# Performance work log

Hardware: AMD Instinct MI355X
Metric: run time of the kernel (lower is better)

The kernel has to match this reference:

```python
import jax, jax.numpy as jnp
import numpy as np

N_HEADS = 16
N_KV_HEADS = 4
HEAD_DIM = 128


def _rope(x, cos, sin):
    # x: [b, s, h, d]; cos/sin: [s, d//2]; interleaved pair rotation
    b, s, h, d = x.shape
    xp = x.reshape(b, s, h, d // 2, 2)
    x_r, x_i = xp[..., 0], xp[..., 1]
    c = cos[None, :, None, :]
    sn = sin[None, :, None, :]
    o_r = x_r * c - x_i * sn
    o_i = x_r * sn + x_i * c
    return jnp.stack([o_r, o_i], axis=-1).reshape(b, s, h, d)


def setup_inputs() -> dict:
    key = jax.random.key(0)
    ks = jax.random.split(key, 7)
    B, S, D = 2, 2048, 2048
    KV = N_KV_HEADS * HEAD_DIM
    x = jax.random.normal(ks[0], (B, S, D), dtype=jnp.float32)
    freqs_cos = jax.random.uniform(ks[1], (S, HEAD_DIM // 2), dtype=jnp.float32)
    freqs_sin = jax.random.uniform(ks[2], (S, HEAD_DIM // 2), dtype=jnp.float32)
    scale = 0.02
    wq = jax.random.normal(ks[3], (D, D), dtype=jnp.float32) * scale
    wk = jax.random.normal(ks[4], (KV, D), dtype=jnp.float32) * scale
    wv = jax.random.normal(ks[5], (KV, D), dtype=jnp.float32) * scale
    wo = jax.random.normal(ks[6], (D, D), dtype=jnp.float32) * scale
    return {"x": x, "freqs_cos": freqs_cos, "freqs_sin": freqs_sin,
            "wq": wq, "wk": wk, "wv": wv, "wo": wo}


def reference(x, freqs_cos, freqs_sin, wq, wk, wv, wo):
    B, S, D = x.shape
    n_rep = N_HEADS // N_KV_HEADS
    q = (x @ wq.T).reshape(B, S, N_HEADS, HEAD_DIM)
    k = (x @ wk.T).reshape(B, S, N_KV_HEADS, HEAD_DIM)
    v = (x @ wv.T).reshape(B, S, N_KV_HEADS, HEAD_DIM)
    q = _rope(q, freqs_cos, freqs_sin)
    k = _rope(k, freqs_cos, freqs_sin)
    # repeat_kv == torch.repeat_interleave along head dim
    k = jnp.repeat(k, n_rep, axis=2)
    v = jnp.repeat(v, n_rep, axis=2)
    q = q.transpose(0, 2, 1, 3)  # [B, H, S, d]
    k = k.transpose(0, 2, 1, 3)
    v = v.transpose(0, 2, 1, 3)
    scale = 1.0 / np.sqrt(HEAD_DIM).astype(np.float32)
    scores = jnp.einsum('bhqd,bhkd->bhqk', q, k) * scale
    causal = jnp.tril(jnp.ones((S, S), dtype=bool))
    scores = jnp.where(causal[None, None], scores, jnp.finfo(jnp.float32).min)
    probs = jax.nn.softmax(scores.astype(jnp.float32), axis=-1).astype(q.dtype)
    out = jnp.einsum('bhqk,bhkd->bhqd', probs, v)
    out = out.transpose(0, 2, 1, 3).reshape(B, S, N_HEADS * HEAD_DIM)
    return out @ wo.T
```

## Files before the change

kernel.cpp:

```cpp
#include <hip/hip_runtime.h>
#include <hip/hip_bf16.h>
#include <type_traits>

using bf16x8 = __attribute__((ext_vector_type(8))) short;
using f32x4  = __attribute__((ext_vector_type(4))) float;
using u16x8  = __attribute__((ext_vector_type(8))) unsigned short;
using u16x4  = __attribute__((ext_vector_type(4))) unsigned short;
using u32x4  = __attribute__((ext_vector_type(4))) unsigned int;

__device__ __forceinline__ float b2f(unsigned short u) {
    unsigned int x = ((unsigned int)u) << 16;
    return __builtin_bit_cast(float, x);
}
__device__ __forceinline__ unsigned short f2b(float f) {
    __hip_bfloat16 h = __float2bfloat16(f);
    return __builtin_bit_cast(unsigned short, h);
}

#if defined(__has_builtin)
#if __has_builtin(__builtin_amdgcn_exp2f)
#define EXP2F(x) __builtin_amdgcn_exp2f(x)
#else
#define EXP2F(x) exp2f(x)
#endif
#else
#define EXP2F(x) exp2f(x)
#endif

__device__ __forceinline__ void async_copy16(const void* g, void* l) {
    __builtin_amdgcn_global_load_lds(
        (const __attribute__((address_space(1))) unsigned int*)g,
        (__attribute__((address_space(3))) unsigned int*)l, 16, 0, 0);
}

#define MFMA16(a, b, c) __builtin_amdgcn_mfma_f32_16x16x32_bf16(a, b, c, 0, 0, 0)

#define BARRIER() do { asm volatile("" ::: "memory"); \
    __builtin_amdgcn_s_barrier(); asm volatile("" ::: "memory"); } while (0)
#define VMCNT6() asm volatile("s_waitcnt vmcnt(6)" ::: "memory")
#define VMCNT0() asm volatile("s_waitcnt vmcnt(0)" ::: "memory")

__global__ __launch_bounds__(256) void cvt_all(
    const float* __restrict__ x,  const float* __restrict__ wq,
    const float* __restrict__ wk, const float* __restrict__ wv,
    const float* __restrict__ wo,
    unsigned short* __restrict__ xb,  unsigned short* __restrict__ wqb,
    unsigned short* __restrict__ wkb, unsigned short* __restrict__ wvb,
    unsigned short* __restrict__ wob)
{
    int i = blockIdx.x * 256 + threadIdx.x;
    const float* s; unsigned short* d; int j;
    if (i < 2097152)      { s = x;  d = xb;  j = i; }
    else if (i < 3145728) { s = wq; d = wqb; j = i - 2097152; }
    else if (i < 3407872) { s = wk; d = wkb; j = i - 3145728; }
    else if (i < 3670016) { s = wv; d = wvb; j = i - 3407872; }
    else                  { s = wo; d = wob; j = i - 3670016; }
    float4 v = ((const float4*)s)[j];
    ushort4 o;
    o.x = f2b(v.x); o.y = f2b(v.y); o.z = f2b(v.z); o.w = f2b(v.w);
    ((ushort4*)d)[j] = o;
}

__global__ __launch_bounds__(512, 2) void qkv_gemm(
    const unsigned short* __restrict__ A,
    const unsigned short* __restrict__ Wq,
    const unsigned short* __restrict__ Wk,
    const unsigned short* __restrict__ Wv,
    const float* __restrict__ fc,
    const float* __restrict__ fs,
    unsigned short* __restrict__ Q,
    unsigned short* __restrict__ Kk,
    unsigned short* __restrict__ V)
{
    const int K = 2048;
    __shared__ unsigned short ldsA[2][256 * 64];
    __shared__ unsigned short ldsB[2][256 * 64];

    int tid  = threadIdx.x;
    int w    = tid >> 6;
    int lane = tid & 63;
    int idx  = lane & 15;
    int quad = lane >> 4;
    int srow   = lane >> 3;
    int schunk = (lane & 7) ^ srow;

    int wfm = (w >> 2) * 64;
    int wfn = (w & 3) * 64;

    int bid = (blockIdx.x & 7) * 24 + (blockIdx.x >> 3);
    int bm = bid / 12;
    int bn = bid - bm * 12;
    int m0 = bm * 256;

    const unsigned short* Bt;
    unsigned short* C;
    int Nc, n0;
    if (bn < 8)       { Bt = Wq + (size_t)bn * 256 * K;        C = Q;  Nc = 2048; n0 = bn * 256; }
    else if (bn < 10) { Bt = Wk + (size_t)(bn - 8) * 256 * K;  C = Kk; Nc = 512;  n0 = (bn - 8) * 256; }
    else              { Bt = Wv + (size_t)(bn - 10) * 256 * K; C = V;  Nc = 512;  n0 = (bn - 10) * 256; }

    const unsigned short* Ab = A + (size_t)m0 * K;

    f32x4 acc[8][4];
    #pragma unroll
    for (int mf = 0; mf < 8; ++mf)
        #pragma unroll
        for (int nf = 0; nf < 4; ++nf) acc[mf][nf] = (f32x4){0.f, 0.f, 0.f, 0.f};

    bf16x8 a[4][2], b0[2][2], b1[2][2];

    auto STAGE = [&](const unsigned short* __restrict__ G, int rb, int kc,
                     unsigned short* dst) {
        #pragma unroll
        for (int i = 0; i < 2; ++i) {
            int R = (w * 2 + i) * 8;
            async_copy16(G + (size_t)(rb + R + srow) * K + kc + schunk * 8,
                         dst + (size_t)R * 64);
        }
    };
    auto LDA = [&](int d, int mh) {
        #pragma unroll
        for (int mi = 0; mi < 4; ++mi) {
            int r = mh * 128 + wfm + mi * 16 + idx;
            #pragma unroll
            for (int ks = 0; ks < 2; ++ks)
                a[mi][ks] = *(const bf16x8*)&ldsA[d][r * 64 + (((ks * 4 + quad) ^ (r & 7)) << 3)];
        }
    };
    auto LDB0 = [&](int d, int nh) {
        #pragma unroll
        for (int nj = 0; nj < 2; ++nj) {
            int r = wfn + nh * 32 + nj * 16 + idx;
            #pragma unroll
            for (int ks = 0; ks < 2; ++ks)
                b0[nj][ks] = *(const bf16x8*)&ldsB[d][r * 64 + (((ks * 4 + quad) ^ (r & 7)) << 3)];
        }
    };
    auto LDB1 = [&](int d, int nh) {
        #pragma unroll
        for (int nj = 0; nj < 2; ++nj) {
            int r = wfn + nh * 32 + nj * 16 + idx;
            #pragma unroll
            for (int ks = 0; ks < 2; ++ks)
                b1[nj][ks] = *(const bf16x8*)&ldsB[d][r * 64 + (((ks * 4 + quad) ^ (r & 7)) << 3)];
        }
    };
    auto MM0 = [&](int mh, int nh) {
        __builtin_amdgcn_s_setprio(1);
        #pragma unroll
        for (int mi = 0; mi < 4; ++mi)
            #pragma unroll
            for (int nj = 0; nj < 2; ++nj)
                #pragma unroll
                for (int ks = 0; ks < 2; ++ks)
                    acc[mh * 4 + mi][nh * 2 + nj] =
                        MFMA16(a[mi][ks], b0[nj][ks], acc[mh * 4 + mi][nh * 2 + nj]);
        __builtin_amdgcn_s_setprio(0);
    };
    auto MM1 = [&](int mh, int nh) {
        __builtin_amdgcn_s_setprio(1);
        #pragma unroll
        for (int mi = 0; mi < 4; ++mi)
            #pragma unroll
            for (int nj = 0; nj < 2; ++nj)
                #pragma unroll
                for (int ks = 0; ks < 2; ++ks)
                    acc[mh * 4 + mi][nh * 2 + nj] =
                        MFMA16(a[mi][ks], b1[nj][ks], acc[mh * 4 + mi][nh * 2 + nj]);
        __builtin_amdgcn_s_setprio(0);
    };

    STAGE(Ab, 0,   0,  &ldsA[0][0]);
    STAGE(Ab, 128, 0,  &ldsA[0][128 * 64]);
    STAGE(Bt, 0,   0,  &ldsB[0][0]);
    STAGE(Bt, 128, 0,  &ldsB[0][128 * 64]);
    STAGE(Ab, 0,   64, &ldsA[1][0]);
    STAGE(Bt, 0,   64, &ldsB[1][0]);
    STAGE(Bt, 128, 64, &ldsB[1][128 * 64]);
    VMCNT6();
    BARRIER();

    for (int it = 0; it < 15; ++it) {
        int u = 2 * it;
        LDA(0, 0); LDB0(0, 0);
        STAGE(Ab, 128, (u + 1) * 64, &ldsA[1][128 * 64]);
        BARRIER(); MM0(0, 0); BARRIER();
        LDB1(0, 1);
        STAGE(Ab, 0, (u + 2) * 64, &ldsA[0][0]);
        BARRIER(); MM1(0, 1); BARRIER();
        LDA(0, 1);
        STAGE(Bt, 0, (u + 2) * 64, &ldsB[0][0]);
        BARRIER(); MM1(1, 1); BARRIER();
        STAGE(Bt, 128, (u + 2) * 64, &ldsB[0][128 * 64]);
        VMCNT6();
        BARRIER(); MM0(1, 0); BARRIER();
        LDA(1, 0); LDB0(1, 0);
        STAGE(Ab, 128, (u + 2) * 64, &ldsA[0][128 * 64]);
        BARRIER(); MM0(0, 0); BARRIER();
        LDB1(1, 1);
        STAGE(Ab, 0, (u + 3) * 64, &ldsA[1][0]);
        BARRIER(); MM1(0, 1); BARRIER();
        LDA(1, 1);
        STAGE(Bt, 0, (u + 3) * 64, &ldsB[1][0]);
        BARRIER(); MM1(1, 1); BARRIER();
        STAGE(Bt, 128, (u + 3) * 64, &ldsB[1][128 * 64]);
        VMCNT6();
        BARRIER(); MM0(1, 0); BARRIER();
    }

    LDA(0, 0); LDB0(0, 0);
    STAGE(Ab, 128, 31 * 64, &ldsA[1][128 * 64]);
    BARRIER(); MM0(0, 0); BARRIER();
    LDB1(0, 1);
    BARRIER(); MM1(0, 1); BARRIER();
    LDA(0, 1);
    BARRIER(); MM1(1, 1); BARRIER();
    VMCNT0();
    BARRIER(); MM0(1, 0); BARRIER();
    LDA(1, 0); LDB0(1, 0);
    BARRIER(); MM0(0, 0); BARRIER();
    LDB1(1, 1);
    BARRIER(); MM1(0, 1); BARRIER();
    LDA(1, 1);
    BARRIER(); MM1(1, 1); BARRIER();
    MM0(1, 0);

    bool dorope = (bn < 10);
    float osc = (bn < 8) ? 0.12752584f : 1.0f;
    #pragma unroll
    for (int mf = 0; mf < 8; ++mf) {
        #pragma unroll
        for (int r = 0; r < 4; ++r) {
            size_t row = (size_t)(m0 + (mf >> 2) * 128 + wfm + (mf & 3) * 16 + quad * 4 + r);
            int srow_ = (int)(row & 2047) * 64;
            #pragma unroll
            for (int nf = 0; nf < 4; ++nf) {
                int col = n0 + wfn + nf * 16 + idx;
                float v = acc[mf][nf][r];
                if (dorope) {
                    float pv = __shfl_xor(v, 1);
                    int fi = srow_ + ((col & 127) >> 1);
                    float c  = fc[fi];
                    float sv = fs[fi];
                    v = (col & 1) ? (pv * sv + v * c) : (v * c - pv * sv);
                    v *= osc;
                }
                C[row * Nc + col] = f2b(v);
            }
        }
    }
}

__device__ __forceinline__ void g_stage(
    const unsigned short* __restrict__ A, const unsigned short* __restrict__ Bt,
    unsigned short* As, unsigned short* Bs,
    int k0, int K, int w, int srow, int schunk)
{
    #pragma unroll
    for (int i = 0; i < 4; ++i) {
        int cb = w * 4 + i;
        size_t goff = (size_t)(cb * 8 + srow) * K + k0 + schunk * 8;
        async_copy16(A  + goff, &As[cb * 512]);
        async_copy16(Bt + goff, &Bs[cb * 512]);
    }
}
__device__ __forceinline__ void g_compute(
    const unsigned short* As, const unsigned short* Bs,
    f32x4 (&acc)[4][4], int wm, int wn, int idx, int quad)
{
    #pragma unroll
    for (int ks = 0; ks < 2; ++ks) {
        bf16x8 af[4], bfr[4];
        #pragma unroll
        for (int mi = 0; mi < 4; ++mi) {
            int row = wm + mi * 16 + idx;
            af[mi] = *(const bf16x8*)&As[row * 64 + (((ks * 4 + quad) ^ (row & 7)) * 8)];
        }
        #pragma unroll
        for (int ni = 0; ni < 4; ++ni) {
            int row = wn + ni * 16 + idx;
            bfr[ni] = *(const bf16x8*)&Bs[row * 64 + (((ks * 4 + quad) ^ (row & 7)) * 8)];
        }
        #pragma unroll
        for (int mi = 0; mi < 4; ++mi)
            #pragma unroll
            for (int ni = 0; ni < 4; ++ni)
                acc[mi][ni] = MFMA16(af[mi], bfr[ni], acc[mi][ni]);
    }
}

template <typename OutT>
__global__ __launch_bounds__(256) void gemm_tile(
    const unsigned short* __restrict__ A,
    const unsigned short* __restrict__ Bt,
    OutT* __restrict__ C,
    int M, int N, int K)
{
    constexpr int BK = 64;
    __shared__ unsigned short As0[128 * BK];
    __shared__ unsigned short Bs0[128 * BK];
    __shared__ unsigned short As1[128 * BK];
    __shared__ unsigned short Bs1[128 * BK];

    int tid  = threadIdx.x;
    int w    = tid >> 6;
    int lane = tid & 63;
    int idx  = lane & 15;
    int quad = lane >> 4;
    int wm   = (w >> 1) * 64;
    int wn   = (w & 1) * 64;

    int tilesN = N / 128;
    int bm = blockIdx.x / tilesN;
    int bn = blockIdx.x - bm * tilesN;
    int m0 = bm * 128, n0 = bn * 128;

    const unsigned short* Ab = A  + (size_t)m0 * K;
    const unsigned short* Bb = Bt + (size_t)n0 * K;

    int srow   = lane >> 3;
    int schunk = (lane & 7) ^ srow;

    f32x4 acc[4][4];
    #pragma unroll
    for (int mi = 0; mi < 4; ++mi)
        #pragma unroll
        for (int ni = 0; ni < 4; ++ni) acc[mi][ni] = (f32x4){0.f, 0.f, 0.f, 0.f};

    g_stage(Ab, Bb, As0, Bs0, 0, K, w, srow, schunk);
    __syncthreads();

    for (int k0 = 0; k0 < K; k0 += 2 * BK) {
        if (k0 + BK < K)
            g_stage(Ab, Bb, As1, Bs1, k0 + BK, K, w, srow, schunk);
        g_compute(As0, Bs0, acc, wm, wn, idx, quad);
        __syncthreads();
        if (k0 + 2 * BK < K)
            g_stage(Ab, Bb, As0, Bs0, k0 + 2 * BK, K, w, srow, schunk);
        g_compute(As1, Bs1, acc, wm, wn, idx, quad);
        __syncthreads();
    }

    #pragma unroll
    for (int mi = 0; mi < 4; ++mi) {
        #pragma unroll
        for (int r = 0; r < 4; ++r) {
            size_t row = (size_t)(m0 + wm + mi * 16 + quad * 4 + r);
            #pragma unroll
            for (int ni = 0; ni < 4; ++ni) {
                int col = n0 + wn + ni * 16 + idx;
                if constexpr (std::is_same_v<OutT, float>) {
                    C[row * N + col] = acc[mi][ni][r];
                } else {
                    C[row * N + col] = f2b(acc[mi][ni][r]);
                }
            }
        }
    }
}

__global__ __launch_bounds__(256, 2) void flash_attn(
    const unsigned short* __restrict__ qg,
    const unsigned short* __restrict__ kk,
    const unsigned short* __restrict__ vv,
    unsigned short* __restrict__ out)
{
    const int S = 2048;
    int bid = blockIdx.x;
    int qp  = bid & 15;
    int bh  = bid >> 4;
    int h   = bh & 15;
    int b   = bh >> 4;
    int kvh = h >> 2;

    int p   = b ? (15 - qp) : qp;

    int tid  = threadIdx.x;
    int w    = tid >> 6;
    int lane = tid & 63;
    int idx  = lane & 15;
    int quad = lane >> 4;

    int qt  = 2 * p + (w >> 1);
    int wq0 = qt * 64 + (w & 1) * 32;
    int qrA = wq0 + idx;

    __shared__ unsigned short Ks[2][64 * 128];
    __shared__ unsigned short Vt[2][128 * 72];

    const unsigned short* kbase = kk + ((size_t)b * S * 4 + kvh) * 128;
    const unsigned short* vbase = vv + ((size_t)b * S * 4 + kvh) * 128;

    bf16x8 qfA[4], qfB[4];
    {
        const unsigned short* qa =
            qg + ((size_t)((b * S + wq0 + idx) * 16 + h)) * 128 + quad * 8;
        const unsigned short* qb2 =
            qg + ((size_t)((b * S + wq0 + 16 + idx) * 16 + h)) * 128 + quad * 8;
        #pragma unroll
        for (int ko = 0; ko < 4; ++ko) {
            qfA[ko] = *(const bf16x8*)(qa  + ko * 32);
            qfB[ko] = *(const bf16x8*)(qb2 + ko * 32);
        }
    }

    f32x4 accA[8], accB[8];
    #pragma unroll
    for (int n = 0; n < 8; ++n) {
        accA[n] = (f32x4){0.f, 0.f, 0.f, 0.f};
        accB[n] = (f32x4){0.f, 0.f, 0.f, 0.f};
    }
    float lsumA = 0.f, lsumB = 0.f;

    int dp = lane * 2;
    int swzslot = ((w ^ ((dp >> 3) & 3)) << 3);

    int nt = 2 * p + 2;

    unsigned int vld[2][8];

    auto STAGE_ISSUE = [&](int t, int d) {
        #pragma unroll
        for (int i = 0; i < 4; ++i) {
            int key = w * 16 + i * 4 + (lane >> 4);
            int sc  = (lane & 15) ^ (key & 7);
            async_copy16(kbase + ((size_t)(t * 64 + key)) * 512 + sc * 8,
                         &Ks[d][(w * 16 + i * 4) * 128]);
        }
        const unsigned short* vc = vbase + ((size_t)t * 64) * 512 + dp;
        #pragma unroll
        for (int hh = 0; hh < 2; ++hh)
            #pragma unroll
            for (int ii = 0; ii < 8; ++ii) {
                int gk = hh * 32 + w * 4 + (ii >> 1) + 16 * (ii & 1);
                vld[hh][ii] = *(const unsigned int*)(vc + (size_t)gk * 512);
            }
    };
    auto STAGE_WRITE = [&](int d) {
        #pragma unroll
        for (int hh = 0; hh < 2; ++hh) {
            u16x8 lo, hi;
            #pragma unroll
            for (int ii = 0; ii < 8; ++ii) {
                lo[ii] = (unsigned short)vld[hh][ii];
                hi[ii] = (unsigned short)(vld[hh][ii] >> 16);
            }
            *(u16x8*)&Vt[d][dp * 72 + hh * 32 + swzslot]       = lo;
            *(u16x8*)&Vt[d][(dp + 1) * 72 + hh * 32 + swzslot] = hi;
        }
    };

    STAGE_ISSUE(0, 0);
    VMCNT0();
    STAGE_WRITE(0);
    __syncthreads();

    for (int t = 0; t < nt; ++t) {
        int bc = t & 1;
        if (t + 1 < nt) STAGE_ISSUE(t + 1, bc ^ 1);

        if (t * 64 <= wq0 + 31) {
            f32x4 sA[4], sB[4];
            #pragma unroll
            for (int g = 0; g < 4; ++g) {
                sA[g] = (f32x4){0.f, 0.f, 0.f, 0.f};
                sB[g] = (f32x4){0.f, 0.f, 0.f, 0.f};
            }
            #pragma unroll
            for (int ko = 0; ko < 4; ++ko) {
                int ch = ((ko * 4 + quad) ^ (idx & 7)) * 8;
                #pragma unroll
                for (int g = 0; g < 4; ++g) {
                    bf16x8 kf = *(const bf16x8*)&Ks[bc][(g * 16 + idx) * 128 + ch];
                    sA[g] = MFMA16(kf, qfA[ko], sA[g]);
                    sB[g] = MFMA16(kf, qfB[ko], sB[g]);
                }
            }
            unsigned int pkA[2][4], pkB[2][4];
            if (t * 64 + 63 <= wq0) {
                #pragma unroll
                for (int hh = 0; hh < 2; ++hh)
                    #pragma unroll
                    for (int r = 0; r < 4; ++r) {
                        float a0 = EXP2F(sA[hh * 2][r]), a1 = EXP2F(sA[hh * 2 + 1][r]);
                        float b0_ = EXP2F(sB[hh * 2][r]), b1_ = EXP2F(sB[hh * 2 + 1][r]);
                        lsumA += a0 + a1;
                        lsumB += b0_ + b1_;
                        pkA[hh][r] = (unsigned int)f2b(a0) | ((unsigned int)f2b(a1) << 16);
                        pkB[hh][r] = (unsigned int)f2b(b0_) | ((unsigned int)f2b(b1_) << 16);
                    }
            } else {
                int LA = qrA - t * 64;
                int LB = LA + 16;
                #pragma unroll
                for (int hh = 0; hh < 2; ++hh)
                    #pragma unroll
                    for (int r = 0; r < 4; ++r) {
                        int kl = hh * 32 + quad * 4 + r;
                        float a0 = (kl      <= LA) ? EXP2F(sA[hh * 2][r]) : 0.f;
                        float a1 = (kl + 16 <= LA) ? EXP2F(sA[hh * 2 + 1][r]) : 0.f;
                        float b0_ = (kl      <= LB) ? EXP2F(sB[hh * 2][r]) : 0.f;
                        float b1_ = (kl + 16 <= LB) ? EXP2F(sB[hh * 2 + 1][r]) : 0.f;
                        lsumA += a0 + a1;
                        lsumB += b0_ + b1_;
                        pkA[hh][r] = (unsigned int)f2b(a0) | ((unsigned int)f2b(a1) << 16);
                        pkB[hh][r] = (unsigned int)f2b(b0_) | ((unsigned int)f2b(b1_) << 16);
                    }
            }
            u32x4 pA0 = {pkA[0][0], pkA[0][1], pkA[0][2], pkA[0][3]};
            u32x4 pA1 = {pkA[1][0], pkA[1][1], pkA[1][2], pkA[1][3]};
            u32x4 pB0 = {pkB[0][0], pkB[0][1], pkB[0][2], pkB[0][3]};
            u32x4 pB1 = {pkB[1][0], pkB[1][1], pkB[1][2], pkB[1][3]};
            bf16x8 pfA0 = __builtin_bit_cast(bf16x8, pA0);
            bf16x8 pfA1 = __builtin_bit_cast(bf16x8, pA1);
            bf16x8 pfB0 = __builtin_bit_cast(bf16x8, pB0);
            bf16x8 pfB1 = __builtin_bit_cast(bf16x8, pB1);
            #pragma unroll
            for (int n = 0; n < 8; ++n) {
                int rr = n * 16 + idx;
                int base = rr * 72 + ((quad ^ ((rr >> 3) & 3)) << 3);
                bf16x8 vf0 = *(const bf16x8*)&Vt[bc][base];
                bf16x8 vf1 = *(const bf16x8*)&Vt[bc][base + 32];
                accA[n] = MFMA16(vf0, pfA0, accA[n]);
                accA[n] = MFMA16(vf1, pfA1, accA[n]);
                accB[n] = MFMA16(vf0, pfB0, accB[n]);
                accB[n] = MFMA16(vf1, pfB1, accB[n]);
            }
        }

        if (t + 1 < nt) {
            VMCNT0();
            STAGE_WRITE(bc ^ 1);
        }
        __syncthreads();
    }

    lsumA += __shfl_xor(lsumA, 16);
    lsumA += __shfl_xor(lsumA, 32);
    lsumB += __shfl_xor(lsumB, 16);
    lsumB += __shfl_xor(lsumB, 32);
    float invA = 1.f / lsumA;
    float invB = 1.f / lsumB;
    size_t rowA = (size_t)(b * S + wq0 + idx) * 2048 + h * 128;
    size_t rowB = rowA + (size_t)16 * 2048;
    #pragma unroll
    for (int n = 0; n < 8; ++n) {
        ushort4 oA, oB;
        oA.x = f2b(accA[n][0] * invA);
        oA.y = f2b(accA[n][1] * invA);
        oA.z = f2b(accA[n][2] * invA);
        oA.w = f2b(accA[n][3] * invA);
        oB.x = f2b(accB[n][0] * invB);
        oB.y = f2b(accB[n][1] * invB);
        oB.z = f2b(accB[n][2] * invB);
        oB.w = f2b(accB[n][3] * invB);
        *(ushort4*)&out[rowA + n * 16 + quad * 4] = oA;
        *(ushort4*)&out[rowB + n * 16 + quad * 4] = oB;
    }
}

extern "C" void kernel_launch(void* const* d_in, const int* in_sizes, int n_in,
                              void* d_out, int out_size, void* d_ws, size_t ws_size,
                              hipStream_t stream)
{
    const float* x  = (const float*)d_in[0];
    const float* fc = (const float*)d_in[1];
    const float* fs = (const float*)d_in[2];
    const float* wq = (const float*)d_in[3];
    const float* wk = (const float*)d_in[4];
    const float* wv = (const float*)d_in[5];
    const float* wo = (const float*)d_in[6];
    float* out = (float*)d_out;

    const int B = 2, S = 2048, D = 2048, KV = 512;
    const int M = B * S;

    unsigned short* ws  = (unsigned short*)d_ws;
    unsigned short* xb  = ws;
    unsigned short* wqb = xb  + (size_t)M * D;
    unsigned short* wkb = wqb + (size_t)D * D;
    unsigned short* wvb = wkb + (size_t)KV * D;
    unsigned short* wob = wvb + (size_t)KV * D;
    unsigned short* qb  = wob + (size_t)D * D;
    unsigned short* kb  = qb  + (size_t)M * D;
    unsigned short* vb  = kb  + (size_t)M * KV;
    unsigned short* ao  = vb  + (size_t)M * KV;

    cvt_all<<<dim3(18432), dim3(256), 0, stream>>>(
        x, wq, wk, wv, wo, xb, wqb, wkb, wvb, wob);

    qkv_gemm<<<dim3(192), dim3(512), 0, stream>>>(
        xb, wqb, wkb, wvb, fc, fs, qb, kb, vb);

    flash_attn<<<dim3(512), dim3(256), 0, stream>>>(qb, kb, vb, ao);

    gemm_tile<float><<<dim3((M / 128) * (D / 128)), dim3(256), 0, stream>>>(ao, wob, out, M, D, D);
}
```

Before: 311.5 us.

## Replace output projection with 256x256 pipelined GEMM and reorder attention block schedule

Replaces the generic 128x128 output-projection GEMM with a specialized 256x256-tile, 512-thread kernel. It interleaves async global-to-LDS staging with split MFMA phases, uses s_setprio around the MFMA bursts, and remaps block indices for cache locality. It also reorders the flash-attention block-to-work mapping so the heaviest causal query tiles are scheduled first across heads and batches. The new GEMM launches only 128 blocks and needs large LDS and register budgets, which may underfill the GPU's compute units.

```diff
diff --git a/kernel.cpp b/kernel.cpp
--- a/kernel.cpp
+++ b/kernel.cpp
@@ -251,109 +251,167 @@
     }
 }
 
-__device__ __forceinline__ void g_stage(
-    const unsigned short* __restrict__ A, const unsigned short* __restrict__ Bt,
-    unsigned short* As, unsigned short* Bs,
-    int k0, int K, int w, int srow, int schunk)
-{
-    #pragma unroll
-    for (int i = 0; i < 4; ++i) {
-        int cb = w * 4 + i;
-        size_t goff = (size_t)(cb * 8 + srow) * K + k0 + schunk * 8;
-        async_copy16(A  + goff, &As[cb * 512]);
-        async_copy16(Bt + goff, &Bs[cb * 512]);
-    }
-}
-__device__ __forceinline__ void g_compute(
-    const unsigned short* As, const unsigned short* Bs,
-    f32x4 (&acc)[4][4], int wm, int wn, int idx, int quad)
-{
-    #pragma unroll
-    for (int ks = 0; ks < 2; ++ks) {
-        bf16x8 af[4], bfr[4];
-        #pragma unroll
-        for (int mi = 0; mi < 4; ++mi) {
-            int row = wm + mi * 16 + idx;
-            af[mi] = *(const bf16x8*)&As[row * 64 + (((ks * 4 + quad) ^ (row & 7)) * 8)];
-        }
-        #pragma unroll
-        for (int ni = 0; ni < 4; ++ni) {
-            int row = wn + ni * 16 + idx;
-            bfr[ni] = *(const bf16x8*)&Bs[row * 64 + (((ks * 4 + quad) ^ (row & 7)) * 8)];
-        }
-        #pragma unroll
-        for (int mi = 0; mi < 4; ++mi)
-            #pragma unroll
-            for (int ni = 0; ni < 4; ++ni)
-                acc[mi][ni] = MFMA16(af[mi], bfr[ni], acc[mi][ni]);
-    }
-}
-
-template <typename OutT>
-__global__ __launch_bounds__(256) void gemm_tile(
+__global__ __launch_bounds__(512, 2) void wo_gemm(
     const unsigned short* __restrict__ A,
     const unsigned short* __restrict__ Bt,
-    OutT* __restrict__ C,
-    int M, int N, int K)
+    float* __restrict__ C)
 {
-    constexpr int BK = 64;
-    __shared__ unsigned short As0[128 * BK];
-    __shared__ unsigned short Bs0[128 * BK];
-    __shared__ unsigned short As1[128 * BK];
-    __shared__ unsigned short Bs1[128 * BK];
+    const int K = 2048;
+    __shared__ unsigned short ldsA[2][256 * 64];
+    __shared__ unsigned short ldsB[2][256 * 64];
 
     int tid  = threadIdx.x;
     int w    = tid >> 6;
     int lane = tid & 63;
     int idx  = lane & 15;
     int quad = lane >> 4;
-    int wm   = (w >> 1) * 64;
-    int wn   = (w & 1) * 64;
-
-    int tilesN = N / 128;
-    int bm = blockIdx.x / tilesN;
-    int bn = blockIdx.x - bm * tilesN;
-    int m0 = bm * 128, n0 = bn * 128;
+    int srow   = lane >> 3;
+    int schunk = (lane & 7) ^ srow;
+
+    int wfm = (w >> 2) * 64;
+    int wfn = (w & 3) * 64;
+
+    int bid = (blockIdx.x & 7) * 16 + (blockIdx.x >> 3);
+    int bm = bid >> 3;
+    int bn = bid & 7;
+    int m0 = bm * 256, n0 = bn * 256;
 
     const unsigned short* Ab = A  + (size_t)m0 * K;
     const unsigned short* Bb = Bt + (size_t)n0 * K;
 
-    int srow   = lane >> 3;
-    int schunk = (lane & 7) ^ srow;
-
-    f32x4 acc[4][4];
+    f32x4 acc[8][4];
     #pragma unroll
-    for (int mi = 0; mi < 4; ++mi)
-        #pragma unroll
-        for (int ni = 0; ni < 4; ++ni) acc[mi][ni] = (f32x4){0.f, 0.f, 0.f, 0.f};
-
-    g_stage(Ab, Bb, As0, Bs0, 0, K, w, srow, schunk);
-    __syncthreads();
-
-    for (int k0 = 0; k0 < K; k0 += 2 * BK) {
-        if (k0 + BK < K)
-            g_stage(Ab, Bb, As1, Bs1, k0 + BK, K, w, srow, schunk);
-        g_compute(As0, Bs0, acc, wm, wn, idx, quad);
-        __syncthreads();
-        if (k0 + 2 * BK < K)
-            g_stage(Ab, Bb, As0, Bs0, k0 + 2 * BK, K, w, srow, schunk);
-        g_compute(As1, Bs1, acc, wm, wn, idx, quad);
-        __syncthreads();
-    }
+    for (int mf = 0; mf < 8; ++mf)
+        #pragma unroll
+        for (int nf = 0; nf < 4; ++nf) acc[mf][nf] = (f32x4){0.f, 0.f, 0.f, 0.f};
+
+    bf16x8 a[4][2], b0[2][2], b1[2][2];
+
+    auto STAGE = [&](const unsigned short* __restrict__ G, int rb, int kc,
+                     unsigned short* dst) {
+        #pragma unroll
+        for (int i = 0; i < 2; ++i) {
+            int R = (w * 2 + i) * 8;
+            async_copy16(G + (size_t)(rb + R + srow) * K + kc + schunk * 8,
+                         dst + (size_t)R * 64);
+        }
+    };
+    auto LDA = [&](int d, int mh) {
+        #pragma unroll
+        for (int mi = 0; mi < 4; ++mi) {
+            int r = mh * 128 + wfm + mi * 16 + idx;
+            #pragma unroll
+            for (int ks = 0; ks < 2; ++ks)
+                a[mi][ks] = *(const bf16x8*)&ldsA[d][r * 64 + (((ks * 4 + quad) ^ (r & 7)) << 3)];
+        }
+    };
+    auto LDB0 = [&](int d, int nh) {
+        #pragma unroll
+        for (int nj = 0; nj < 2; ++nj) {
+            int r = wfn + nh * 32 + nj * 16 + idx;
+            #pragma unroll
+            for (int ks = 0; ks < 2; ++ks)
+                b0[nj][ks] = *(const bf16x8*)&ldsB[d][r * 64 + (((ks * 4 + quad) ^ (r & 7)) << 3)];
+        }
+    };
+    auto LDB1 = [&](int d, int nh) {
+        #pragma unroll
+        for (int nj = 0; nj < 2; ++nj) {
+            int r = wfn + nh * 32 + nj * 16 + idx;
+            #pragma unroll
+            for (int ks = 0; ks < 2; ++ks)
+                b1[nj][ks] = *(const bf16x8*)&ldsB[d][r * 64 + (((ks * 4 + quad) ^ (r & 7)) << 3)];
+        }
+    };
+    auto MM0 = [&](int mh, int nh) {
+        __builtin_amdgcn_s_setprio(1);
+        #pragma unroll
+        for (int mi = 0; mi < 4; ++mi)
+            #pragma unroll
+            for (int nj = 0; nj < 2; ++nj)
+                #pragma unroll
+                for (int ks = 0; ks < 2; ++ks)
+                    acc[mh * 4 + mi][nh * 2 + nj] =
+                        MFMA16(a[mi][ks], b0[nj][ks], acc[mh * 4 + mi][nh * 2 + nj]);
+        __builtin_amdgcn_s_setprio(0);
+    };
+    auto MM1 = [&](int mh, int nh) {
+        __builtin_amdgcn_s_setprio(1);
+        #pragma unroll
+        for (int mi = 0; mi < 4; ++mi)
+            #pragma unroll
+            for (int nj = 0; nj < 2; ++nj)
+                #pragma unroll
+                for (int ks = 0; ks < 2; ++ks)
+                    acc[mh * 4 + mi][nh * 2 + nj] =
+                        MFMA16(a[mi][ks], b1[nj][ks], acc[mh * 4 + mi][nh * 2 + nj]);
+        __builtin_amdgcn_s_setprio(0);
+    };
+
+    STAGE(Ab, 0,   0,  &ldsA[0][0]);
+    STAGE(Ab, 128, 0,  &ldsA[0][128 * 64]);
+    STAGE(Bb, 0,   0,  &ldsB[0][0]);
+    STAGE(Bb, 128, 0,  &ldsB[0][128 * 64]);
+    STAGE(Ab, 0,   64, &ldsA[1][0]);
+    STAGE(Bb, 0,   64, &ldsB[1][0]);
+    STAGE(Bb, 128, 64, &ldsB[1][128 * 64]);
+    VMCNT6();
+    BARRIER();
+
+    for (int it = 0; it < 15; ++it) {
+        int u = 2 * it;
+        LDA(0, 0); LDB0(0, 0);
+        STAGE(Ab, 128, (u + 1) * 64, &ldsA[1][128 * 64]);
+        BARRIER(); MM0(0, 0); BARRIER();
+        LDB1(0, 1);
+        STAGE(Ab, 0, (u + 2) * 64, &ldsA[0][0]);
+        BARRIER(); MM1(0, 1); BARRIER();
+        LDA(0, 1);
+        STAGE(Bb, 0, (u + 2) * 64, &ldsB[0][0]);
+        BARRIER(); MM1(1, 1); BARRIER();
+        STAGE(Bb, 128, (u + 2) * 64, &ldsB[0][128 * 64]);
+        VMCNT6();
+        BARRIER(); MM0(1, 0); BARRIER();
+        LDA(1, 0); LDB0(1, 0);
+        STAGE(Ab, 128, (u + 2) * 64, &ldsA[0][128 * 64]);
+        BARRIER(); MM0(0, 0); BARRIER();
+        LDB1(1, 1);
+        STAGE(Ab, 0, (u + 3) * 64, &ldsA[1][0]);
+        BARRIER(); MM1(0, 1); BARRIER();
+        LDA(1, 1);
+        STAGE(Bb, 0, (u + 3) * 64, &ldsB[1][0]);
+        BARRIER(); MM1(1, 1); BARRIER();
+        STAGE(Bb, 128, (u + 3) * 64, &ldsB[1][128 * 64]);
+        VMCNT6();
+        BARRIER(); MM0(1, 0); BARRIER();
+    }
+
+    LDA(0, 0); LDB0(0, 0);
+    STAGE(Ab, 128, 31 * 64, &ldsA[1][128 * 64]);
+    BARRIER(); MM0(0, 0); BARRIER();
+    LDB1(0, 1);
+    BARRIER(); MM1(0, 1); BARRIER();
+    LDA(0, 1);
+    BARRIER(); MM1(1, 1); BARRIER();
+    VMCNT0();
+    BARRIER(); MM0(1, 0); BARRIER();
+    LDA(1, 0); LDB0(1, 0);
+    BARRIER(); MM0(0, 0); BARRIER();
+    LDB1(1, 1);
+    BARRIER(); MM1(0, 1); BARRIER();
+    LDA(1, 1);
+    BARRIER(); MM1(1, 1); BARRIER();
+    MM0(1, 0);
 
     #pragma unroll
-    for (int mi = 0; mi < 4; ++mi) {
+    for (int mf = 0; mf < 8; ++mf) {
         #pragma unroll
         for (int r = 0; r < 4; ++r) {
-            size_t row = (size_t)(m0 + wm + mi * 16 + quad * 4 + r);
-            #pragma unroll
-            for (int ni = 0; ni < 4; ++ni) {
-                int col = n0 + wn + ni * 16 + idx;
-                if constexpr (std::is_same_v<OutT, float>) {
-                    C[row * N + col] = acc[mi][ni][r];
-                } else {
-                    C[row * N + col] = f2b(acc[mi][ni][r]);
-                }
+            size_t row = (size_t)(m0 + (mf >> 2) * 128 + wfm + (mf & 3) * 16 + quad * 4 + r);
+            #pragma unroll
+            for (int nf = 0; nf < 4; ++nf) {
+                int col = n0 + wfn + nf * 16 + idx;
+                C[row * 2048 + col] = acc[mf][nf][r];
             }
         }
     }
@@ -367,13 +425,13 @@
 {
     const int S = 2048;
     int bid = blockIdx.x;
-    int qp  = bid & 15;
-    int bh  = bid >> 4;
-    int h   = bh & 15;
-    int b   = bh >> 4;
+    int grp = bid >> 8;
+    int i_  = bid & 255;
+    int b   = i_ & 1;
+    int h   = (i_ >> 1) & 15;
+    int pp  = i_ >> 5;
+    int p   = grp ? pp : (15 - pp);
     int kvh = h >> 2;
-
-    int p   = b ? (15 - qp) : qp;
 
     int tid  = threadIdx.x;
     int w    = tid >> 6;
@@ -594,5 +652,5 @@
 
     flash_attn<<<dim3(512), dim3(256), 0, stream>>>(qb, kb, vb, ao);
 
-    gemm_tile<float><<<dim3((M / 128) * (D / 128)), dim3(256), 0, stream>>>(ao, wob, out, M, D, D);
-}
+    wo_gemm<<<dim3(128), dim3(512), 0, stream>>>(ao, wob, out);
+}
```

Result: slower. 330.2 us (+6.0%).
